# Kernel optimization log

Measured on AMD Instinct MI355X. Metric: run time of the kernel, lower is better.

The kernel has to match this reference:

```python
import jax, jax.numpy as jnp
import numpy as np
from math import sqrt

B, IN_C, OUT_C, H, W, WDIM, K = 16, 512, 512, 64, 64, 512, 3
EPS = 1e-8
LRELU_SLOPE = 0.2


def setup_inputs() -> dict:
    key = jax.random.key(0)
    ks = jax.random.split(key, 5)
    return {
        "x": jax.random.normal(ks[0], (B, IN_C, H, W), dtype=jnp.float32),
        "w": jax.random.normal(ks[1], (B, WDIM), dtype=jnp.float32),
        "noise": jax.random.normal(ks[2], (B, 1, H, W), dtype=jnp.float32),
        "linear_w": jax.random.normal(ks[3], (IN_C, WDIM), dtype=jnp.float32),
        "linear_b": jnp.ones((IN_C,), dtype=jnp.float32),
        "conv_w": jax.random.normal(ks[4], (OUT_C, IN_C, K, K), dtype=jnp.float32),
        "scale_noise": jnp.zeros((OUT_C,), dtype=jnp.float32),
        "bias": jnp.zeros((OUT_C,), dtype=jnp.float32),
    }


def reference(x, w, noise, linear_w, linear_b, conv_w, scale_noise, bias):
    # EqualizerStraights: equalized-lr linear, scale = 1/sqrt(w_dim)
    s = w @ (linear_w * (1.0 / sqrt(WDIM))).T + linear_b  # [b, in_c]
    # Weight_Demod: equalized conv weight, scale = 1/sqrt(in_c*k*k)
    base_w = conv_w * (1.0 / sqrt(IN_C * K * K))  # [out, in, k, k]
    weights = base_w[None] * s[:, None, :, None, None]  # [b, out, in, k, k]
    sigma_inv = jax.lax.rsqrt(
        jnp.sum(weights * weights, axis=(2, 3, 4), keepdims=True) + EPS)
    weights = weights * sigma_inv

    def conv1(xi, wi):  # xi [in,h,w], wi [out,in,k,k]
        return jax.lax.conv_general_dilated(
            xi[None], wi, window_strides=(1, 1), padding="SAME",
            dimension_numbers=("NCHW", "OIHW", "NCHW"))[0]

    y = jax.vmap(conv1)(x, weights)  # [b, out, h, w]
    y = y + scale_noise[None, :, None, None] * noise
    return jax.nn.leaky_relu(y + bias[None, :, None, None], negative_slope=LRELU_SLOPE)
```

## Files before the change

### kernel.cpp

```cpp
#include <hip/hip_runtime.h>
#include <hip/hip_bf16.h>
#include <stdint.h>

typedef __bf16 bf16_t;
typedef __bf16 bf16x8 __attribute__((ext_vector_type(8)));
typedef short short8 __attribute__((ext_vector_type(8)));
typedef float f32x4 __attribute__((ext_vector_type(4)));

#define RS512  0.044194173824159216f
#define RS4608 0.014731391274719739f

__global__ void k_style(const float* __restrict__ w, const float* __restrict__ lw,
                        const float* __restrict__ lb, float* __restrict__ s) {
  int b = blockIdx.y;
  int c = blockIdx.x * 256 + threadIdx.x;
  const float4* wr = (const float4*)(w + b * 512);
  const float4* lr = (const float4*)(lw + (size_t)c * 512);
  float acc = 0.f;
#pragma unroll 4
  for (int d = 0; d < 128; ++d) {
    float4 a = wr[d], q = lr[d];
    acc += a.x * q.x + a.y * q.y + a.z * q.z + a.w * q.w;
  }
  s[b * 512 + c] = acc * RS512 + lb[c];
}

__global__ void k_wprep(const float* __restrict__ cw, float* __restrict__ wsq,
                        bf16_t* __restrict__ bwf, f32x4* __restrict__ zb) {
  if (blockIdx.x == 0) zb[threadIdx.x] = (f32x4)0.f;
  int idx = blockIdx.x * 256 + threadIdx.x;
  int o = idx >> 9, i = idx & 511;
  float v[9];
  float ss = 0.f;
#pragma unroll
  for (int t = 0; t < 9; ++t) {
    float x = cw[(size_t)idx * 9 + t] * RS4608;
    v[t] = x;
    ss += x * x;
  }
  wsq[idx] = ss;
  int lane = (o & 15) | (((i >> 3) & 3) << 4);
  int base_blk = (i >> 5) * 32 + (o >> 4);
#pragma unroll
  for (int t = 0; t < 9; ++t) {
    size_t e = ((size_t)(t * 512 + base_blk) << 9) + lane * 8 + (i & 7);
    bwf[e] = (bf16_t)v[t];
  }
}

__global__ void k_sigma(const float* __restrict__ s, const float* __restrict__ wsq,
                        float* __restrict__ sinv) {
  __shared__ float s2[512];
  int b = blockIdx.y;
  int o = blockIdx.x * 256 + threadIdx.x;
  for (int i = threadIdx.x; i < 512; i += 256) {
    float v = s[b * 512 + i];
    s2[i] = v * v;
  }
  __syncthreads();
  const float4* qr = (const float4*)(wsq + (size_t)o * 512);
  float acc = 0.f;
#pragma unroll 4
  for (int d = 0; d < 128; ++d) {
    float4 q = qr[d];
    acc += q.x * s2[4 * d] + q.y * s2[4 * d + 1] + q.z * s2[4 * d + 2] + q.w * s2[4 * d + 3];
  }
  sinv[b * 512 + o] = rsqrtf(acc + 1e-8f);
}

__global__ void k_xt(const float* __restrict__ x, const float* __restrict__ s,
                     bf16_t* __restrict__ xt) {
  int ic = blockIdx.x, h = blockIdx.y, b = blockIdx.z;
  __shared__ __align__(16) bf16_t tile[8192];
  int t = threadIdx.x;
  int wcol = t & 63;
  int g = t >> 6;
#pragma unroll
  for (int blk = 0; blk < 4; ++blk) {
    int grp = blk * 4 + g;
    bf16x8 vec;
#pragma unroll
    for (int k = 0; k < 8; ++k) {
      int i = ic * 128 + grp * 8 + k;
      float v = x[(((size_t)b * 512 + i) * 64 + h) * 64 + wcol] * s[b * 512 + i];
      vec[k] = (bf16_t)v;
    }
    int chunk = grp ^ (wcol & 15);
    *(bf16x8*)((char*)tile + wcol * 256 + chunk * 16) = vec;
  }
  __syncthreads();
#pragma unroll
  for (int j = 0; j < 4; ++j) {
    int flat = j * 256 + t;
    int wo = flat >> 4, ig8 = flat & 15;
    int chunk = ig8 ^ (wo & 15);
    bf16x8 v = *(bf16x8*)((char*)tile + wo * 256 + chunk * 16);
    int c32 = (ig8 >> 2);
    int slot = (ig8 & 3) ^ ((wo >> 1) & 3);
    *(bf16x8*)(xt + (((size_t)b * 64 + h) * 64 + wo) * 512 + ic * 128 + c32 * 32 + slot * 8) = v;
  }
}

#define AS1 __attribute__((address_space(1)))
#define AS3 __attribute__((address_space(3)))

__device__ __forceinline__ void gl16(const void* g, void* l) {
  __builtin_amdgcn_global_load_lds((const AS1 void*)g, (AS3 void*)l, 16, 0, 0);
}

#define VMCNT(n) asm volatile("s_waitcnt vmcnt(" #n ")" ::: "memory")
#define BAR __builtin_amdgcn_s_barrier()

__global__ __launch_bounds__(512, 4) void k_conv(
    const bf16_t* __restrict__ xt, const bf16_t* __restrict__ bwf,
    const float* __restrict__ sinv, const float* __restrict__ noise,
    const float* __restrict__ snz, const float* __restrict__ bias,
    const char* __restrict__ zb, float* __restrict__ out) {
  __shared__ __align__(16) char lds[73728];

  const int t = threadIdx.x;
  const int rq = blockIdx.x;
  const int OY = blockIdx.y;
  const int b = blockIdx.z;
  const int h0 = rq * 4;
  const int lane = t & 63;
  const int wv = t >> 6;
  const int wm = wv & 1;
  const int wn = wv >> 1;

  const char* xg = (const char*)xt + (size_t)b * 4194304 + (lane >> 2) * 1024 + (lane & 3) * 16;
  const char* wgsrc = (const char*)bwf + ((OY * 8 + wv) << 10) + (lane << 4);

  f32x4 acc[4][4] = {};

  const char* xsrc[3];
  uint32_t xdst[3];
#pragma unroll
  for (int k = 0; k < 3; ++k) {
    int slot = wv * 3 + k, row = slot >> 2, q = slot & 3;
    int gr = h0 - 1 + row;
    bool valid = (unsigned)gr < 64u;
    xsrc[k] = valid ? (xg + (size_t)gr * 65536 + q * 16384) : (zb + lane * 16);
    xdst[k] = (uint32_t)(24576 + row * 4096 + q * 1024);
  }

  const uint32_t woff = (uint32_t)((wm << 12) + (lane << 4));
  uint32_t pX[4][3];
#pragma unroll
  for (int j = 0; j < 4; ++j)
#pragma unroll
    for (int dk = 0; dk < 3; ++dk) {
      int icol = j * 16 + (lane & 15) + dk - 1;
      int ic2 = icol < 0 ? 0 : (icol > 63 ? 63 : icol);
      int slot = (lane >> 4) ^ ((ic2 >> 1) & 3);
      pX[j][dk] = (uint32_t)(24576 + wn * 4096 + ic2 * 64 + slot * 16);
    }
  const bool c0 = (lane & 15) == 0;
  const bool c15 = (lane & 15) == 15;

  auto stW = [&](uint32_t srcoff, int slab) {
    gl16(wgsrc + srcoff, lds + slab * 8192 + (wv << 10));
  };
  auto stX = [&](int k, uint32_t cxoff, int xb) {
    gl16(xsrc[k] + cxoff, lds + xdst[k] + (uint32_t)(xb * 24576));
  };

  auto COMP = [&](int JC, int XB) {
    const int ky = JC / 3, kx = JC % 3;
    bf16x8 af[4];
#pragma unroll
    for (int mi = 0; mi < 4; ++mi)
      af[mi] = *(const bf16x8*)(lds + (uint32_t)((JC % 3) * 8192) + woff + (uint32_t)(mi * 1024));
    bf16x8 bfr[4];
#pragma unroll
    for (int col = 0; col < 4; ++col) {
      short8 xv = *(const short8*)(lds + pX[col][kx] +
                                   (uint32_t)(XB * 24576 + ky * 4096));
      if (kx == 0 && col == 0) xv = c0 ? (short8)0 : xv;
      if (kx == 2 && col == 3) xv = c15 ? (short8)0 : xv;
      bfr[col] = __builtin_bit_cast(bf16x8, xv);
    }
    __builtin_amdgcn_s_setprio(1);
#pragma unroll
    for (int mi = 0; mi < 4; ++mi)
#pragma unroll
      for (int col = 0; col < 4; ++col)
        acc[mi][col] =
            __builtin_amdgcn_mfma_f32_16x16x32_bf16(af[mi], bfr[col], acc[mi][col], 0, 0, 0);
    __builtin_amdgcn_s_setprio(0);
  };

#define PHASE(CWB, CXB, JC, LAST, XB)                                          \
  {                                                                            \
    if ((JC) + 2 <= 8) stW((CWB) + (uint32_t)((JC) + 2) * 524288u, ((JC) + 2) % 3); \
    else if (!(LAST)) stW((CWB) + 32768u + (uint32_t)((JC) - 7) * 524288u, ((JC) + 2) % 3); \
    if (!(LAST) && (JC) < 3) stX((JC), (CXB), (XB) ^ 1);                       \
    if (LAST) {                                                                \
      if ((JC) <= 6) { VMCNT(2); }                                             \
      else if ((JC) == 7) { VMCNT(1); }                                        \
      else { VMCNT(0); }                                                       \
    } else {                                                                   \
      if ((JC) == 0 || (JC) == 4) { VMCNT(3); }                                \
      else if ((JC) == 1 || (JC) == 3) { VMCNT(4); }                           \
      else if ((JC) == 2) { VMCNT(5); }                                        \
      else { VMCNT(2); }                                                       \
    }                                                                          \
    __builtin_amdgcn_s_barrier();                                              \
    COMP((JC), (XB));                                                          \
  }

#pragma unroll
  for (int k = 0; k < 3; ++k) stX(k, 0u, 0);
  stW(0u, 0);
  stW(524288u, 1);
  VMCNT(0); BAR;

  uint32_t cwb = 0, cxb = 64;
#pragma unroll 1
  for (int ci = 0; ci < 7; ++ci) {
#pragma unroll
    for (int jc = 0; jc < 9; ++jc) PHASE(cwb, cxb, jc, 0, 0);
    cwb += 32768u; cxb += 64u;
#pragma unroll
    for (int jc = 0; jc < 9; ++jc) PHASE(cwb, cxb, jc, 0, 1);
    cwb += 32768u; cxb += 64u;
  }
#pragma unroll
  for (int jc = 0; jc < 9; ++jc) PHASE(cwb, cxb, jc, 0, 0);
  cwb += 32768u;
#pragma unroll
  for (int jc = 0; jc < 9; ++jc) PHASE(cwb, 0u, jc, 1, 1);

  const float* sb = sinv + b * 512;
  const int og = OY * 128 + wm * 64 + ((lane >> 4) << 2);
  const int colb = lane & 15;
  const int prow = h0 + wn;
  float nzv[4];
#pragma unroll
  for (int col = 0; col < 4; ++col)
    nzv[col] = noise[(size_t)b * 4096 + prow * 64 + col * 16 + colb];
#pragma unroll
  for (int mi = 0; mi < 4; ++mi) {
#pragma unroll
    for (int r = 0; r < 4; ++r) {
      int o = og + mi * 16 + r;
      float sv = sb[o];
      float nw = snz[o];
      float bv = bias[o];
      float* orow = out + (((size_t)b * 512 + o) * 64 + prow) * 64;
#pragma unroll
      for (int col = 0; col < 4; ++col) {
        float v = acc[mi][col][r] * sv + nw * nzv[col] + bv;
        orow[col * 16 + colb] = v > 0.f ? v : 0.2f * v;
      }
    }
  }
}

extern "C" void kernel_launch(void* const* d_in, const int* in_sizes, int n_in,
                              void* d_out, int out_size, void* d_ws, size_t ws_size,
                              hipStream_t stream) {
  const float* x     = (const float*)d_in[0];
  const float* w     = (const float*)d_in[1];
  const float* noise = (const float*)d_in[2];
  const float* lw    = (const float*)d_in[3];
  const float* lb    = (const float*)d_in[4];
  const float* cw    = (const float*)d_in[5];
  const float* snz   = (const float*)d_in[6];
  const float* bias  = (const float*)d_in[7];
  float* out = (float*)d_out;

  char* ws = (char*)d_ws;
  bf16_t* xt   = (bf16_t*)ws;
  bf16_t* bwf  = (bf16_t*)(ws + 67108864);
  float*  s    = (float*)(ws + 71827456);
  float*  sinv = (float*)(ws + 71860224);
  float*  wsq  = (float*)(ws + 71892992);
  char*   zbuf = ws + 72941568;

  k_style<<<dim3(2, 16), 256, 0, stream>>>(w, lw, lb, s);
  k_wprep<<<dim3(1024), 256, 0, stream>>>(cw, wsq, bwf, (f32x4*)zbuf);
  k_sigma<<<dim3(2, 16), 256, 0, stream>>>(s, wsq, sinv);
  k_xt<<<dim3(4, 64, 16), 256, 0, stream>>>(x, s, xt);
  k_conv<<<dim3(16, 4, 16), 512, 0, stream>>>(xt, bwf, sinv, noise, snz, bias, zbuf, out);
}
```

Before: 302.8 us.

## Load conv weights directly into registers and relayout activation tiles

Weight fragments now go straight from global memory into double-buffered registers (wA/wB) instead of being staged through LDS, which shrinks LDS from 72KB to about 49KB. The per-tap barriers and vmcnt waits are replaced by one __syncthreads per input-channel chunk. The activation transpose layout changes to a k-group-major form so B-operand addresses are linear offsets, and the zero buffer moves to the start of the workspace so source offsets become uniform scalars. The risks are higher VGPR pressure from the extra register buffers and weight loads that are no longer shared across waves, which adds redundant global and L2 traffic.

Measured after the change: 312.3 us. 3.1% more time.

```diff
diff --git a/kernel.cpp b/kernel.cpp
--- a/kernel.cpp
+++ b/kernel.cpp
@@ -95,9 +95,10 @@
     int wo = flat >> 4, ig8 = flat & 15;
     int chunk = ig8 ^ (wo & 15);
     bf16x8 v = *(bf16x8*)((char*)tile + wo * 256 + chunk * 16);
-    int c32 = (ig8 >> 2);
-    int slot = (ig8 & 3) ^ ((wo >> 1) & 3);
-    *(bf16x8*)(xt + (((size_t)b * 64 + h) * 64 + wo) * 512 + ic * 128 + c32 * 32 + slot * 8) = v;
+    int cc = ic * 4 + (ig8 >> 2);
+    int kgr = ig8 & 3;
+    size_t dst = ((((size_t)b * 64 + h) * 16 + cc) << 11) + (kgr << 9) + (size_t)wo * 8;
+    *(bf16x8*)(xt + dst) = v;
   }
 }
 
@@ -108,15 +109,15 @@
   __builtin_amdgcn_global_load_lds((const AS1 void*)g, (AS3 void*)l, 16, 0, 0);
 }
 
-#define VMCNT(n) asm volatile("s_waitcnt vmcnt(" #n ")" ::: "memory")
-#define BAR __builtin_amdgcn_s_barrier()
+#define XT0 4096u
 
 __global__ __launch_bounds__(512, 4) void k_conv(
-    const bf16_t* __restrict__ xt, const bf16_t* __restrict__ bwf,
+    const char* __restrict__ wsb,
+    const bf16_t* __restrict__ bwf,
     const float* __restrict__ sinv, const float* __restrict__ noise,
     const float* __restrict__ snz, const float* __restrict__ bias,
-    const char* __restrict__ zb, float* __restrict__ out) {
-  __shared__ __align__(16) char lds[73728];
+    float* __restrict__ out) {
+  __shared__ __align__(16) char lds[50176];
 
   const int t = threadIdx.x;
   const int rq = blockIdx.x;
@@ -128,108 +129,89 @@
   const int wm = wv & 1;
   const int wn = wv >> 1;
 
-  const char* xg = (const char*)xt + (size_t)b * 4194304 + (lane >> 2) * 1024 + (lane & 3) * 16;
-  const char* wgsrc = (const char*)bwf + ((OY * 8 + wv) << 10) + (lane << 4);
-
   f32x4 acc[4][4] = {};
-
-  const char* xsrc[3];
-  uint32_t xdst[3];
+  bf16x8 wA[4], wB[4];
+
+  uint32_t xsoff[3], xdst[3], xsel[3];
 #pragma unroll
   for (int k = 0; k < 3; ++k) {
     int slot = wv * 3 + k, row = slot >> 2, q = slot & 3;
     int gr = h0 - 1 + row;
-    bool valid = (unsigned)gr < 64u;
-    xsrc[k] = valid ? (xg + (size_t)gr * 65536 + q * 16384) : (zb + lane * 16);
-    xdst[k] = (uint32_t)(24576 + row * 4096 + q * 1024);
-  }
-
-  const uint32_t woff = (uint32_t)((wm << 12) + (lane << 4));
-  uint32_t pX[4][3];
-#pragma unroll
-  for (int j = 0; j < 4; ++j)
-#pragma unroll
-    for (int dk = 0; dk < 3; ++dk) {
-      int icol = j * 16 + (lane & 15) + dk - 1;
-      int ic2 = icol < 0 ? 0 : (icol > 63 ? 63 : icol);
-      int slot = (lane >> 4) ^ ((ic2 >> 1) & 3);
-      pX[j][dk] = (uint32_t)(24576 + wn * 4096 + ic2 * 64 + slot * 16);
-    }
+    int valid = ((unsigned)gr < 64u) ? 1 : 0;
+    uint32_t so = valid ? (XT0 + (uint32_t)b * 4194304u + (uint32_t)gr * 65536u +
+                           (uint32_t)q * 1024u)
+                        : 0u;
+    xsoff[k] = __builtin_amdgcn_readfirstlane(so);
+    xdst[k] = __builtin_amdgcn_readfirstlane((uint32_t)(1024 + row * 4096 + q * 1024));
+    xsel[k] = __builtin_amdgcn_readfirstlane((uint32_t)valid);
+  }
+
+  auto stX = [&](int k, uint32_t cxoff, int xb) {
+    uint32_t co = xsel[k] ? cxoff : 0u;
+    gl16(wsb + xsoff[k] + co + (size_t)(lane * 16), lds + xdst[k] + (uint32_t)(xb * 24576));
+  };
+
+  const size_t wbase0 = ((size_t)(OY * 8 + wm * 4)) << 10;
+  auto loadW = [&](int tap, int c, bf16x8* d) {
+    const char* p = (const char*)bwf + wbase0 + (((size_t)(tap * 16 + c)) << 15);
+#pragma unroll
+    for (int mi = 0; mi < 4; ++mi)
+      d[mi] = *(const bf16x8*)(p + mi * 1024 + (size_t)(lane * 16));
+  };
+
+  const uint32_t pXbase =
+      (uint32_t)(1024 + wn * 4096 + (lane >> 4) * 1024 + (lane & 15) * 16);
   const bool c0 = (lane & 15) == 0;
   const bool c15 = (lane & 15) == 15;
 
-  auto stW = [&](uint32_t srcoff, int slab) {
-    gl16(wgsrc + srcoff, lds + slab * 8192 + (wv << 10));
-  };
-  auto stX = [&](int k, uint32_t cxoff, int xb) {
-    gl16(xsrc[k] + cxoff, lds + xdst[k] + (uint32_t)(xb * 24576));
-  };
-
-  auto COMP = [&](int JC, int XB) {
-    const int ky = JC / 3, kx = JC % 3;
-    bf16x8 af[4];
-#pragma unroll
-    for (int mi = 0; mi < 4; ++mi)
-      af[mi] = *(const bf16x8*)(lds + (uint32_t)((JC % 3) * 8192) + woff + (uint32_t)(mi * 1024));
-    bf16x8 bfr[4];
-#pragma unroll
-    for (int col = 0; col < 4; ++col) {
-      short8 xv = *(const short8*)(lds + pX[col][kx] +
-                                   (uint32_t)(XB * 24576 + ky * 4096));
-      if (kx == 0 && col == 0) xv = c0 ? (short8)0 : xv;
-      if (kx == 2 && col == 3) xv = c15 ? (short8)0 : xv;
-      bfr[col] = __builtin_bit_cast(bf16x8, xv);
-    }
-    __builtin_amdgcn_s_setprio(1);
-#pragma unroll
-    for (int mi = 0; mi < 4; ++mi)
-#pragma unroll
-      for (int col = 0; col < 4; ++col)
-        acc[mi][col] =
-            __builtin_amdgcn_mfma_f32_16x16x32_bf16(af[mi], bfr[col], acc[mi][col], 0, 0, 0);
-    __builtin_amdgcn_s_setprio(0);
-  };
-
-#define PHASE(CWB, CXB, JC, LAST, XB)                                          \
+#define CTAP(J, XB, AF)                                                        \
   {                                                                            \
-    if ((JC) + 2 <= 8) stW((CWB) + (uint32_t)((JC) + 2) * 524288u, ((JC) + 2) % 3); \
-    else if (!(LAST)) stW((CWB) + 32768u + (uint32_t)((JC) - 7) * 524288u, ((JC) + 2) % 3); \
-    if (!(LAST) && (JC) < 3) stX((JC), (CXB), (XB) ^ 1);                       \
-    if (LAST) {                                                                \
-      if ((JC) <= 6) { VMCNT(2); }                                             \
-      else if ((JC) == 7) { VMCNT(1); }                                        \
-      else { VMCNT(0); }                                                       \
-    } else {                                                                   \
-      if ((JC) == 0 || (JC) == 4) { VMCNT(3); }                                \
-      else if ((JC) == 1 || (JC) == 3) { VMCNT(4); }                           \
-      else if ((JC) == 2) { VMCNT(5); }                                        \
-      else { VMCNT(2); }                                                       \
+    const int ky = (J) / 3, kx = (J) % 3;                                      \
+    __builtin_amdgcn_s_setprio(1);                                             \
+    _Pragma("unroll") for (int col = 0; col < 4; ++col) {                      \
+      short8 xv = *(const short8*)(lds + pXbase +                              \
+                                   (uint32_t)((XB) * 24576 + ky * 4096 +       \
+                                              col * 256 + (kx - 1) * 16));     \
+      if (kx == 0 && col == 0) xv = c0 ? (short8)0 : xv;                       \
+      if (kx == 2 && col == 3) xv = c15 ? (short8)0 : xv;                      \
+      bf16x8 bv = __builtin_bit_cast(bf16x8, xv);                              \
+      _Pragma("unroll") for (int mi = 0; mi < 4; ++mi)                         \
+          acc[mi][col] = __builtin_amdgcn_mfma_f32_16x16x32_bf16(              \
+              AF[mi], bv, acc[mi][col], 0, 0, 0);                              \
     }                                                                          \
-    __builtin_amdgcn_s_barrier();                                              \
-    COMP((JC), (XB));                                                          \
+    __builtin_amdgcn_s_setprio(0);                                             \
+  }
+
+#define CHUNK(C, XB, P, LAST)                                                  \
+  {                                                                            \
+    _Pragma("unroll") for (int j = 0; j < 9; ++j) {                            \
+      if (!(LAST) && j < 3) stX(j, (uint32_t)(((C) + 1) * 4096), (XB) ^ 1);    \
+      if (j < 8) {                                                             \
+        if (((j + (P)) & 1) == 0) loadW(j + 1, (C), wB);                       \
+        else loadW(j + 1, (C), wA);                                            \
+      } else if (!(LAST)) {                                                    \
+        if (((j + (P)) & 1) == 0) loadW(0, (C) + 1, wB);                       \
+        else loadW(0, (C) + 1, wA);                                            \
+      }                                                                        \
+      if (((j + (P)) & 1) == 0) CTAP(j, (XB), wA)                              \
+      else CTAP(j, (XB), wB)                                                   \
+    }                                                                          \
+    __syncthreads();                                                           \
   }
 
 #pragma unroll
   for (int k = 0; k < 3; ++k) stX(k, 0u, 0);
-  stW(0u, 0);
-  stW(524288u, 1);
-  VMCNT(0); BAR;
-
-  uint32_t cwb = 0, cxb = 64;
+  loadW(0, 0, wA);
+  __syncthreads();
+
 #pragma unroll 1
   for (int ci = 0; ci < 7; ++ci) {
-#pragma unroll
-    for (int jc = 0; jc < 9; ++jc) PHASE(cwb, cxb, jc, 0, 0);
-    cwb += 32768u; cxb += 64u;
-#pragma unroll
-    for (int jc = 0; jc < 9; ++jc) PHASE(cwb, cxb, jc, 0, 1);
-    cwb += 32768u; cxb += 64u;
-  }
-#pragma unroll
-  for (int jc = 0; jc < 9; ++jc) PHASE(cwb, cxb, jc, 0, 0);
-  cwb += 32768u;
-#pragma unroll
-  for (int jc = 0; jc < 9; ++jc) PHASE(cwb, 0u, jc, 1, 1);
+    const int c = ci * 2;
+    CHUNK(c, 0, 0, 0);
+    CHUNK(c + 1, 1, 1, 0);
+  }
+  CHUNK(14, 0, 0, 0);
+  CHUNK(15, 1, 1, 1);
 
   const float* sb = sinv + b * 512;
   const int og = OY * 128 + wm * 64 + ((lane >> 4) << 2);
@@ -271,16 +253,16 @@
   float* out = (float*)d_out;
 
   char* ws = (char*)d_ws;
-  bf16_t* xt   = (bf16_t*)ws;
-  bf16_t* bwf  = (bf16_t*)(ws + 67108864);
-  float*  s    = (float*)(ws + 71827456);
-  float*  sinv = (float*)(ws + 71860224);
-  float*  wsq  = (float*)(ws + 71892992);
-  char*   zbuf = ws + 72941568;
+  char*   zbuf = ws;
+  bf16_t* xt   = (bf16_t*)(ws + 4096);
+  bf16_t* bwf  = (bf16_t*)(ws + 67112960);
+  float*  s    = (float*)(ws + 71831552);
+  float*  sinv = (float*)(ws + 71864320);
+  float*  wsq  = (float*)(ws + 71897088);
 
   k_style<<<dim3(2, 16), 256, 0, stream>>>(w, lw, lb, s);
   k_wprep<<<dim3(1024), 256, 0, stream>>>(cw, wsq, bwf, (f32x4*)zbuf);
   k_sigma<<<dim3(2, 16), 256, 0, stream>>>(s, wsq, sinv);
   k_xt<<<dim3(4, 64, 16), 256, 0, stream>>>(x, s, xt);
-  k_conv<<<dim3(16, 4, 16), 512, 0, stream>>>(xt, bwf, sinv, noise, snz, bias, zbuf, out);
-}
+  k_conv<<<dim3(16, 4, 16), 512, 0, stream>>>(ws, bwf, sinv, noise, snz, bias, out);
+}
```

## Reuse center-tap LDS fragment for left/right taps via DPP lane shifts

Applied to the files above, without the earlier changes.

Reorders the nine conv taps per row so the center tap (kx=1) is computed first and its B-operand fragments stay in registers. The left and right taps are then formed by DPP row rotations across the 16-lane column groups, with neighbour-column stitching and zeroing at image edges. This replaces the kx=0 and kx=2 LDS reads, cutting B-fragment LDS traffic to a third. In exchange it adds DPP moves and selects, reorders the weight-slab prefetch sequence to match, and routes out-of-range input rows to a fixed zero-buffer offset.

Result: slower. 320.9 us (+6.0%).

```diff
diff --git a/kernel.cpp b/kernel.cpp
--- a/kernel.cpp
+++ b/kernel.cpp
@@ -6,6 +6,7 @@
 typedef __bf16 bf16x8 __attribute__((ext_vector_type(8)));
 typedef short short8 __attribute__((ext_vector_type(8)));
 typedef float f32x4 __attribute__((ext_vector_type(4)));
+typedef int int4v __attribute__((ext_vector_type(4)));
 
 #define RS512  0.044194173824159216f
 #define RS4608 0.014731391274719739f
@@ -111,6 +112,33 @@
 #define VMCNT(n) asm volatile("s_waitcnt vmcnt(" #n ")" ::: "memory")
 #define BAR __builtin_amdgcn_s_barrier()
 
+#define CONSP(p) (((p) % 3 == 0) ? (p) + 1 : (((p) % 3 == 1) ? (p) - 1 : (p)))
+
+__device__ __forceinline__ int4v dpp_ror1(int4v v) {
+  int4v r;
+  r[0] = __builtin_amdgcn_mov_dpp(v[0], 0x121, 0xf, 0xf, true);
+  r[1] = __builtin_amdgcn_mov_dpp(v[1], 0x121, 0xf, 0xf, true);
+  r[2] = __builtin_amdgcn_mov_dpp(v[2], 0x121, 0xf, 0xf, true);
+  r[3] = __builtin_amdgcn_mov_dpp(v[3], 0x121, 0xf, 0xf, true);
+  return r;
+}
+__device__ __forceinline__ int4v dpp_rol1(int4v v) {
+  int4v r;
+  r[0] = __builtin_amdgcn_mov_dpp(v[0], 0x12F, 0xf, 0xf, true);
+  r[1] = __builtin_amdgcn_mov_dpp(v[1], 0x12F, 0xf, 0xf, true);
+  r[2] = __builtin_amdgcn_mov_dpp(v[2], 0x12F, 0xf, 0xf, true);
+  r[3] = __builtin_amdgcn_mov_dpp(v[3], 0x12F, 0xf, 0xf, true);
+  return r;
+}
+__device__ __forceinline__ int4v sel4(bool c, int4v a, int4v b) {
+  int4v r;
+  r[0] = c ? a[0] : b[0];
+  r[1] = c ? a[1] : b[1];
+  r[2] = c ? a[2] : b[2];
+  r[3] = c ? a[3] : b[3];
+  return r;
+}
+
 __global__ __launch_bounds__(512, 4) void k_conv(
     const bf16_t* __restrict__ xt, const bf16_t* __restrict__ bwf,
     const float* __restrict__ sinv, const float* __restrict__ noise,
@@ -132,9 +160,10 @@
   const char* wgsrc = (const char*)bwf + ((OY * 8 + wv) << 10) + (lane << 4);
 
   f32x4 acc[4][4] = {};
+  int4v F[4];
 
   const char* xsrc[3];
-  uint32_t xdst[3];
+  uint32_t xdst[3], xsel[3];
 #pragma unroll
   for (int k = 0; k < 3; ++k) {
     int slot = wv * 3 + k, row = slot >> 2, q = slot & 3;
@@ -142,19 +171,17 @@
     bool valid = (unsigned)gr < 64u;
     xsrc[k] = valid ? (xg + (size_t)gr * 65536 + q * 16384) : (zb + lane * 16);
     xdst[k] = (uint32_t)(24576 + row * 4096 + q * 1024);
+    xsel[k] = valid ? 1u : 0u;
   }
 
   const uint32_t woff = (uint32_t)((wm << 12) + (lane << 4));
-  uint32_t pX[4][3];
-#pragma unroll
-  for (int j = 0; j < 4; ++j)
-#pragma unroll
-    for (int dk = 0; dk < 3; ++dk) {
-      int icol = j * 16 + (lane & 15) + dk - 1;
-      int ic2 = icol < 0 ? 0 : (icol > 63 ? 63 : icol);
-      int slot = (lane >> 4) ^ ((ic2 >> 1) & 3);
-      pX[j][dk] = (uint32_t)(24576 + wn * 4096 + ic2 * 64 + slot * 16);
-    }
+  uint32_t pXc[4];
+#pragma unroll
+  for (int j = 0; j < 4; ++j) {
+    int icol = j * 16 + (lane & 15);
+    int slot = (lane >> 4) ^ ((icol >> 1) & 3);
+    pXc[j] = (uint32_t)(24576 + wn * 4096 + icol * 64 + slot * 16);
+  }
   const bool c0 = (lane & 15) == 0;
   const bool c15 = (lane & 15) == 15;
 
@@ -162,74 +189,109 @@
     gl16(wgsrc + srcoff, lds + slab * 8192 + (wv << 10));
   };
   auto stX = [&](int k, uint32_t cxoff, int xb) {
-    gl16(xsrc[k] + cxoff, lds + xdst[k] + (uint32_t)(xb * 24576));
+    uint32_t co = xsel[k] ? cxoff : 0u;
+    gl16(xsrc[k] + co, lds + xdst[k] + (uint32_t)(xb * 24576));
   };
 
-  auto COMP = [&](int JC, int XB) {
-    const int ky = JC / 3, kx = JC % 3;
-    bf16x8 af[4];
-#pragma unroll
-    for (int mi = 0; mi < 4; ++mi)
-      af[mi] = *(const bf16x8*)(lds + (uint32_t)((JC % 3) * 8192) + woff + (uint32_t)(mi * 1024));
-    bf16x8 bfr[4];
-#pragma unroll
-    for (int col = 0; col < 4; ++col) {
-      short8 xv = *(const short8*)(lds + pX[col][kx] +
-                                   (uint32_t)(XB * 24576 + ky * 4096));
-      if (kx == 0 && col == 0) xv = c0 ? (short8)0 : xv;
-      if (kx == 2 && col == 3) xv = c15 ? (short8)0 : xv;
-      bfr[col] = __builtin_bit_cast(bf16x8, xv);
-    }
-    __builtin_amdgcn_s_setprio(1);
-#pragma unroll
-    for (int mi = 0; mi < 4; ++mi)
-#pragma unroll
-      for (int col = 0; col < 4; ++col)
-        acc[mi][col] =
-            __builtin_amdgcn_mfma_f32_16x16x32_bf16(af[mi], bfr[col], acc[mi][col], 0, 0, 0);
-    __builtin_amdgcn_s_setprio(0);
-  };
-
-#define PHASE(CWB, CXB, JC, LAST, XB)                                          \
+#define LOAD_AF(SLAB)                                                          \
+  bf16x8 af[4];                                                                \
+  _Pragma("unroll") for (int mi = 0; mi < 4; ++mi)                             \
+      af[mi] = *(const bf16x8*)(lds + (uint32_t)((SLAB) * 8192) + woff +       \
+                                (uint32_t)(mi * 1024));
+
+#define CPH_C(SLAB, KY, XB)                                                    \
   {                                                                            \
-    if ((JC) + 2 <= 8) stW((CWB) + (uint32_t)((JC) + 2) * 524288u, ((JC) + 2) % 3); \
-    else if (!(LAST)) stW((CWB) + 32768u + (uint32_t)((JC) - 7) * 524288u, ((JC) + 2) % 3); \
-    if (!(LAST) && (JC) < 3) stX((JC), (CXB), (XB) ^ 1);                       \
+    LOAD_AF(SLAB)                                                              \
+    _Pragma("unroll") for (int col = 0; col < 4; ++col)                        \
+        F[col] = *(const int4v*)(lds + pXc[col] +                              \
+                                 (uint32_t)((XB) * 24576 + (KY) * 4096));      \
+    __builtin_amdgcn_s_setprio(1);                                             \
+    _Pragma("unroll") for (int mi = 0; mi < 4; ++mi)                           \
+        _Pragma("unroll") for (int col = 0; col < 4; ++col)                    \
+            acc[mi][col] = __builtin_amdgcn_mfma_f32_16x16x32_bf16(            \
+                af[mi], __builtin_bit_cast(bf16x8, F[col]), acc[mi][col],      \
+                0, 0, 0);                                                      \
+    __builtin_amdgcn_s_setprio(0);                                             \
+  }
+
+#define CPH_L(SLAB)                                                            \
+  {                                                                            \
+    LOAD_AF(SLAB)                                                              \
+    __builtin_amdgcn_s_setprio(1);                                             \
+    int4v gp = (int4v)0;                                                       \
+    _Pragma("unroll") for (int col = 0; col < 4; ++col) {                      \
+      int4v g = dpp_ror1(F[col]);                                              \
+      int4v bv = sel4(c0, gp, g);                                              \
+      _Pragma("unroll") for (int mi = 0; mi < 4; ++mi)                         \
+          acc[mi][col] = __builtin_amdgcn_mfma_f32_16x16x32_bf16(              \
+              af[mi], __builtin_bit_cast(bf16x8, bv), acc[mi][col], 0, 0, 0);  \
+      gp = g;                                                                  \
+    }                                                                          \
+    __builtin_amdgcn_s_setprio(0);                                             \
+  }
+
+#define CPH_R(SLAB)                                                            \
+  {                                                                            \
+    LOAD_AF(SLAB)                                                              \
+    __builtin_amdgcn_s_setprio(1);                                             \
+    int4v gn = (int4v)0;                                                       \
+    _Pragma("unroll") for (int cr_ = 0; cr_ < 4; ++cr_) {                      \
+      const int col = 3 - cr_;                                                 \
+      int4v g = dpp_rol1(F[col]);                                              \
+      int4v bv = sel4(c15, gn, g);                                             \
+      _Pragma("unroll") for (int mi = 0; mi < 4; ++mi)                         \
+          acc[mi][col] = __builtin_amdgcn_mfma_f32_16x16x32_bf16(              \
+              af[mi], __builtin_bit_cast(bf16x8, bv), acc[mi][col], 0, 0, 0);  \
+      gn = g;                                                                  \
+    }                                                                          \
+    __builtin_amdgcn_s_setprio(0);                                             \
+  }
+
+#define PHASE(CWB, CXB, P, LAST, XB)                                           \
+  {                                                                            \
+    if ((P) + 2 <= 8)                                                          \
+      stW((CWB) + (uint32_t)(CONSP((P) + 2)) * 524288u, CONSP((P) + 2) % 3);   \
+    else if (!(LAST))                                                          \
+      stW((CWB) + 32768u + (uint32_t)(CONSP((P) - 7)) * 524288u,               \
+          CONSP((P) - 7) % 3);                                                 \
+    if (!(LAST) && (P) < 3) stX((P), (CXB), (XB) ^ 1);                         \
     if (LAST) {                                                                \
-      if ((JC) <= 6) { VMCNT(2); }                                             \
-      else if ((JC) == 7) { VMCNT(1); }                                        \
+      if ((P) <= 6) { VMCNT(2); }                                              \
+      else if ((P) == 7) { VMCNT(1); }                                         \
       else { VMCNT(0); }                                                       \
     } else {                                                                   \
-      if ((JC) == 0 || (JC) == 4) { VMCNT(3); }                                \
-      else if ((JC) == 1 || (JC) == 3) { VMCNT(4); }                           \
-      else if ((JC) == 2) { VMCNT(5); }                                        \
+      if ((P) == 0 || (P) == 4) { VMCNT(3); }                                  \
+      else if ((P) == 1 || (P) == 3) { VMCNT(4); }                             \
+      else if ((P) == 2) { VMCNT(5); }                                         \
       else { VMCNT(2); }                                                       \
     }                                                                          \
     __builtin_amdgcn_s_barrier();                                              \
-    COMP((JC), (XB));                                                          \
+    if ((P) % 3 == 0) CPH_C(CONSP(P) % 3, (P) / 3, XB)                         \
+    else if ((P) % 3 == 1) CPH_L(CONSP(P) % 3)                                 \
+    else CPH_R(CONSP(P) % 3)                                                   \
   }
 
 #pragma unroll
   for (int k = 0; k < 3; ++k) stX(k, 0u, 0);
+  stW(524288u, 1);
   stW(0u, 0);
-  stW(524288u, 1);
   VMCNT(0); BAR;
 
   uint32_t cwb = 0, cxb = 64;
 #pragma unroll 1
   for (int ci = 0; ci < 7; ++ci) {
 #pragma unroll
-    for (int jc = 0; jc < 9; ++jc) PHASE(cwb, cxb, jc, 0, 0);
+    for (int p = 0; p < 9; ++p) PHASE(cwb, cxb, p, 0, 0);
     cwb += 32768u; cxb += 64u;
 #pragma unroll
-    for (int jc = 0; jc < 9; ++jc) PHASE(cwb, cxb, jc, 0, 1);
+    for (int p = 0; p < 9; ++p) PHASE(cwb, cxb, p, 0, 1);
     cwb += 32768u; cxb += 64u;
   }
 #pragma unroll
-  for (int jc = 0; jc < 9; ++jc) PHASE(cwb, cxb, jc, 0, 0);
+  for (int p = 0; p < 9; ++p) PHASE(cwb, cxb, p, 0, 0);
   cwb += 32768u;
 #pragma unroll
-  for (int jc = 0; jc < 9; ++jc) PHASE(cwb, 0u, jc, 1, 1);
+  for (int p = 0; p < 9; ++p) PHASE(cwb, 0u, p, 1, 1);
 
   const float* sb = sinv + b * 512;
   const int og = OY * 128 + wm * 64 + ((lane >> 4) << 2);
```
